# Kernel optimization log

Measured on AMD Instinct MI355X. Metric: run time of the kernel, lower is better.

## Reference

```python
import jax, jax.numpy as jnp
import numpy as np

B, S, DIM = 4, 2048, 1024
H, HD = 16, 64
MB = 16
NMB = S // MB
DEG, CP = 3, 8
NB = CP + DEG  # 11 basis functions
NKNOTS = CP + 1 + 2 * DEG  # 15
EPS = 1e-6
BASE_LR = 1.0


def bspline(x, knots, degree=DEG):
    # Cox-de Boor recursion; x: (...,), knots: (G,) uniform -> (..., G-1-degree)
    xk = x[..., None]
    G = knots.shape[0]
    b = ((xk >= knots[:-1]) & (xk < knots[1:])).astype(x.dtype)
    for k in range(1, degree + 1):
        left = (xk - knots[: G - 1 - k]) / (knots[k: G - 1] - knots[: G - 1 - k])
        right = (knots[k + 1: G] - xk) / (knots[k + 1: G] - knots[1: G - k])
        b = left * b[..., :-1] + right * b[..., 1:]
    return b


def ln_fwd(x, gamma, beta, eps=EPS):
    mu = x.mean(-1, keepdims=True)
    var = ((x - mu) ** 2).mean(-1, keepdims=True)
    x_hat = (x - mu) / jnp.sqrt(var + eps)
    return gamma * x_hat + beta


def ln_fused_l2_bwd(x, l2_target, gamma, beta, eps=EPS):
    mu = x.mean(-1, keepdims=True)
    var = ((x - mu) ** 2).mean(-1, keepdims=True)
    std = jnp.sqrt(var + eps)
    x_hat = (x - mu) / std
    grad_x_hat = (gamma * x_hat + beta - l2_target) * gamma
    z = (grad_x_hat - grad_x_hat.mean(-1, keepdims=True)
         - x_hat * (grad_x_hat * x_hat).mean(-1, keepdims=True)) / std
    return z


def apply_rope(t, ang):
    # t: (B,H,S,hd), ang: (S, hd//2) rotation angles
    cos, sin = jnp.cos(ang), jnp.sin(ang)
    t1, t2 = t[..., 0::2], t[..., 1::2]
    r1 = t1 * cos - t2 * sin
    r2 = t1 * sin + t2 * cos
    return jnp.stack([r1, r2], axis=-1).reshape(t.shape)


def setup_inputs() -> dict:
    key = jax.random.key(0)
    ks = jax.random.split(key, 8)
    s = 0.02
    x = jax.random.normal(ks[0], (B, S, DIM), dtype=jnp.float32)
    inv_freq = 1.0 / (10000.0 ** (jnp.arange(0, HD, 2, dtype=jnp.float32) / HD))
    pos_frequencies = jnp.arange(S, dtype=jnp.float32)[:, None] * inv_freq[None, :]
    Wq = jax.random.normal(ks[1], (DIM, DIM), dtype=jnp.float32) * s
    Wk = jax.random.normal(ks[2], (DIM, DIM), dtype=jnp.float32) * s
    Wv = jax.random.normal(ks[3], (DIM, DIM), dtype=jnp.float32) * s
    Wo = jax.random.normal(ks[4], (DIM, DIM), dtype=jnp.float32) * s
    lr_W = jax.random.normal(ks[5], (H, 1, DIM), dtype=jnp.float32) * s
    lr_b = jnp.zeros((H, 1), dtype=jnp.float32)
    g_scale = jnp.zeros((MB,), dtype=jnp.float32)
    ttt_gamma = jnp.ones((H, HD), dtype=jnp.float32)
    ttt_beta = jnp.zeros((H, HD), dtype=jnp.float32)
    post_w = jnp.ones((DIM,), dtype=jnp.float32)
    post_b = jnp.zeros((DIM,), dtype=jnp.float32)
    knots = jnp.linspace(-1.0, 1.0, NKNOTS, dtype=jnp.float32)
    coefficients = jax.random.normal(ks[6], (H, NB, HD), dtype=jnp.float32) * s
    return dict(x=x, pos_frequencies=pos_frequencies, Wq=Wq, Wk=Wk, Wv=Wv, Wo=Wo,
                lr_W=lr_W, lr_b=lr_b, g_scale=g_scale, ttt_gamma=ttt_gamma,
                ttt_beta=ttt_beta, post_w=post_w, post_b=post_b,
                coefficients=coefficients, knots=knots)


def reference(x, pos_frequencies, Wq, Wk, Wv, Wo, lr_W, lr_b, g_scale,
              ttt_gamma, ttt_beta, post_w, post_b, coefficients, knots):
    Bx, Sx = x.shape[:2]
    proj = lambda W: (x @ W.T).reshape(Bx, Sx, H, HD).transpose(0, 2, 1, 3)
    Q = apply_rope(proj(Wq), pos_frequencies)
    K = apply_rope(proj(Wk), pos_frequencies)
    V = apply_rope(proj(Wv), pos_frequencies)

    to_mb = lambda t: t.reshape(Bx, H, NMB, MB, HD).transpose(2, 0, 1, 3, 4)
    Qm, Km, Vm = to_mb(Q), to_mb(K), to_mb(V)  # (n,B,H,m,hd)

    # inner-loop learning rates (get_learning_rate)
    x4 = x.reshape(Bx, NMB, MB, DIM)
    lr = BASE_LR * jax.nn.sigmoid(
        jnp.einsum('bnkd,hd->bhnk', x4, lr_W[:, 0, :]) + lr_b.reshape(1, H, 1, 1)) / HD
    gs = jnp.clip(1.0 / jnp.arange(1, MB + 1, dtype=x.dtype) + g_scale, 0.0, None)
    eta = (lr * gs).transpose(2, 0, 1, 3)  # (n,B,H,m)

    gamma = ttt_gamma[None, :, None, :]
    beta = ttt_beta[None, :, None, :]
    W0 = jnp.broadcast_to(coefficients, (Bx, H, NB, HD))

    def step(W, inp):
        Qi, Ki, Vi, ei = inp  # (B,H,m,hd), eta (B,H,m)
        basK = bspline(Ki, knots)                      # (B,H,m,hd,nb)
        Zk = jax.nn.silu(Ki) + jnp.einsum('bhmdn,bhnd->bhmd', basK, W)
        gz = ln_fused_l2_bwd(Zk, Vi - Ki, gamma, beta)  # (B,H,m,hd)
        tok = jnp.einsum('bhm,bhmd,bhmdn->bhmnd', ei, gz, basK)
        cum = jnp.cumsum(tok, axis=2)                  # causal coeff-grad (B,H,m,nb,hd)
        basQ = bspline(Qi, knots)
        Zq = (jax.nn.silu(Qi)
              + jnp.einsum('bhmdn,bhnd->bhmd', basQ, W)
              - jnp.einsum('bhmdn,bhmnd->bhmd', basQ, cum))
        y = Qi + ln_fwd(Zq, gamma, beta)
        return W - cum[:, :, -1], y

    _, ys = jax.lax.scan(step, W0, (Qm, Km, Vm, eta))  # ys: (n,B,H,m,hd)
    out = ys.transpose(1, 0, 3, 2, 4).reshape(Bx, Sx, DIM)

    mu = out.mean(-1, keepdims=True)
    var = ((out - mu) ** 2).mean(-1, keepdims=True)
    out = (out - mu) / jnp.sqrt(var + EPS) * post_w + post_b
    return out @ Wo.T
```

## Files before the change

### kernel.cpp

```cpp
#include <hip/hip_runtime.h>
#include <stdint.h>


typedef unsigned short ushort_t;
typedef _Float16 f16x8 __attribute__((ext_vector_type(8)));
typedef float f32x4 __attribute__((ext_vector_type(4)));

__device__ __forceinline__ float bf2f(ushort_t u) {
    union { uint32_t i; float f; } v; v.i = ((uint32_t)u) << 16; return v.f;
}

__device__ __forceinline__ float fast_silu(float x) {
    const float e = __builtin_amdgcn_exp2f(-1.4426950408889634f * x);
    return x * __builtin_amdgcn_rcpf(1.0f + e);
}
__device__ __forceinline__ float fast_rsq(float x) {
    return __builtin_amdgcn_rsqf(x);
}

__device__ __forceinline__ void gl16(const ushort_t* g, ushort_t* l) {
    __builtin_amdgcn_global_load_lds(
        (const __attribute__((address_space(1))) void*)g,
        (__attribute__((address_space(3))) void*)l, 16, 0, 0);
}

template <int CTRL>
__device__ __forceinline__ float dpp_add(float v) {
    int p = __builtin_amdgcn_update_dpp(0, __float_as_int(v), CTRL, 0xF, 0xF, false);
    return v + __int_as_float(p);
}
__device__ __forceinline__ float wave_sum(float v) {
    v = dpp_add<0xB1>(v);
    v = dpp_add<0x4E>(v);
    v = dpp_add<0x141>(v);
    v = dpp_add<0x140>(v);
    v = dpp_add<0x142>(v);
    v = dpp_add<0x143>(v);
    return __int_as_float(__builtin_amdgcn_readlane(__float_as_int(v), 63));
}

__device__ __forceinline__ float rdl63(float v) {
    return __int_as_float(__builtin_amdgcn_readlane(__float_as_int(v), 63));
}

__device__ __forceinline__ void wave_sum6(float& s0, float& s1, float& s2,
                                          float& s3, float& s4, float& s5) {
    asm volatile(
        "s_nop 1\n\t"
        "v_add_f32_dpp %0, %0, %0 quad_perm:[1,0,3,2] row_mask:0xf bank_mask:0xf\n\t"
        "v_add_f32_dpp %1, %1, %1 quad_perm:[1,0,3,2] row_mask:0xf bank_mask:0xf\n\t"
        "v_add_f32_dpp %2, %2, %2 quad_perm:[1,0,3,2] row_mask:0xf bank_mask:0xf\n\t"
        "v_add_f32_dpp %3, %3, %3 quad_perm:[1,0,3,2] row_mask:0xf bank_mask:0xf\n\t"
        "v_add_f32_dpp %4, %4, %4 quad_perm:[1,0,3,2] row_mask:0xf bank_mask:0xf\n\t"
        "v_add_f32_dpp %5, %5, %5 quad_perm:[1,0,3,2] row_mask:0xf bank_mask:0xf\n\t"
        "v_add_f32_dpp %0, %0, %0 quad_perm:[2,3,0,1] row_mask:0xf bank_mask:0xf\n\t"
        "v_add_f32_dpp %1, %1, %1 quad_perm:[2,3,0,1] row_mask:0xf bank_mask:0xf\n\t"
        "v_add_f32_dpp %2, %2, %2 quad_perm:[2,3,0,1] row_mask:0xf bank_mask:0xf\n\t"
        "v_add_f32_dpp %3, %3, %3 quad_perm:[2,3,0,1] row_mask:0xf bank_mask:0xf\n\t"
        "v_add_f32_dpp %4, %4, %4 quad_perm:[2,3,0,1] row_mask:0xf bank_mask:0xf\n\t"
        "v_add_f32_dpp %5, %5, %5 quad_perm:[2,3,0,1] row_mask:0xf bank_mask:0xf\n\t"
        "v_add_f32_dpp %0, %0, %0 row_half_mirror row_mask:0xf bank_mask:0xf\n\t"
        "v_add_f32_dpp %1, %1, %1 row_half_mirror row_mask:0xf bank_mask:0xf\n\t"
        "v_add_f32_dpp %2, %2, %2 row_half_mirror row_mask:0xf bank_mask:0xf\n\t"
        "v_add_f32_dpp %3, %3, %3 row_half_mirror row_mask:0xf bank_mask:0xf\n\t"
        "v_add_f32_dpp %4, %4, %4 row_half_mirror row_mask:0xf bank_mask:0xf\n\t"
        "v_add_f32_dpp %5, %5, %5 row_half_mirror row_mask:0xf bank_mask:0xf\n\t"
        "v_add_f32_dpp %0, %0, %0 row_mirror row_mask:0xf bank_mask:0xf\n\t"
        "v_add_f32_dpp %1, %1, %1 row_mirror row_mask:0xf bank_mask:0xf\n\t"
        "v_add_f32_dpp %2, %2, %2 row_mirror row_mask:0xf bank_mask:0xf\n\t"
        "v_add_f32_dpp %3, %3, %3 row_mirror row_mask:0xf bank_mask:0xf\n\t"
        "v_add_f32_dpp %4, %4, %4 row_mirror row_mask:0xf bank_mask:0xf\n\t"
        "v_add_f32_dpp %5, %5, %5 row_mirror row_mask:0xf bank_mask:0xf\n\t"
        "v_add_f32_dpp %0, %0, %0 row_bcast:15 row_mask:0xf bank_mask:0xf bound_ctrl:0\n\t"
        "v_add_f32_dpp %1, %1, %1 row_bcast:15 row_mask:0xf bank_mask:0xf bound_ctrl:0\n\t"
        "v_add_f32_dpp %2, %2, %2 row_bcast:15 row_mask:0xf bank_mask:0xf bound_ctrl:0\n\t"
        "v_add_f32_dpp %3, %3, %3 row_bcast:15 row_mask:0xf bank_mask:0xf bound_ctrl:0\n\t"
        "v_add_f32_dpp %4, %4, %4 row_bcast:15 row_mask:0xf bank_mask:0xf bound_ctrl:0\n\t"
        "v_add_f32_dpp %5, %5, %5 row_bcast:15 row_mask:0xf bank_mask:0xf bound_ctrl:0\n\t"
        "v_add_f32_dpp %0, %0, %0 row_bcast:31 row_mask:0xf bank_mask:0xf bound_ctrl:0\n\t"
        "v_add_f32_dpp %1, %1, %1 row_bcast:31 row_mask:0xf bank_mask:0xf bound_ctrl:0\n\t"
        "v_add_f32_dpp %2, %2, %2 row_bcast:31 row_mask:0xf bank_mask:0xf bound_ctrl:0\n\t"
        "v_add_f32_dpp %3, %3, %3 row_bcast:31 row_mask:0xf bank_mask:0xf bound_ctrl:0\n\t"
        "v_add_f32_dpp %4, %4, %4 row_bcast:31 row_mask:0xf bank_mask:0xf bound_ctrl:0\n\t"
        "v_add_f32_dpp %5, %5, %5 row_bcast:31 row_mask:0xf bank_mask:0xf bound_ctrl:0"
        : "+v"(s0), "+v"(s1), "+v"(s2), "+v"(s3), "+v"(s4), "+v"(s5));
}

__device__ __forceinline__ void wave_sum2(float& s0, float& s1) {
    asm volatile(
        "s_nop 1\n\t"
        "v_add_f32_dpp %0, %0, %0 quad_perm:[1,0,3,2] row_mask:0xf bank_mask:0xf\n\t"
        "v_add_f32_dpp %1, %1, %1 quad_perm:[1,0,3,2] row_mask:0xf bank_mask:0xf\n\t"
        "s_nop 0\n\t"
        "v_add_f32_dpp %0, %0, %0 quad_perm:[2,3,0,1] row_mask:0xf bank_mask:0xf\n\t"
        "v_add_f32_dpp %1, %1, %1 quad_perm:[2,3,0,1] row_mask:0xf bank_mask:0xf\n\t"
        "s_nop 0\n\t"
        "v_add_f32_dpp %0, %0, %0 row_half_mirror row_mask:0xf bank_mask:0xf\n\t"
        "v_add_f32_dpp %1, %1, %1 row_half_mirror row_mask:0xf bank_mask:0xf\n\t"
        "s_nop 0\n\t"
        "v_add_f32_dpp %0, %0, %0 row_mirror row_mask:0xf bank_mask:0xf\n\t"
        "v_add_f32_dpp %1, %1, %1 row_mirror row_mask:0xf bank_mask:0xf\n\t"
        "s_nop 0\n\t"
        "v_add_f32_dpp %0, %0, %0 row_bcast:15 row_mask:0xf bank_mask:0xf bound_ctrl:0\n\t"
        "v_add_f32_dpp %1, %1, %1 row_bcast:15 row_mask:0xf bank_mask:0xf bound_ctrl:0\n\t"
        "s_nop 0\n\t"
        "v_add_f32_dpp %0, %0, %0 row_bcast:31 row_mask:0xf bank_mask:0xf bound_ctrl:0\n\t"
        "v_add_f32_dpp %1, %1, %1 row_bcast:31 row_mask:0xf bank_mask:0xf bound_ctrl:0"
        : "+v"(s0), "+v"(s1));
}

struct Bas4 { float n[4]; int row; };
__device__ __forceinline__ Bas4 bspline4(float x) {
    const float xp1 = x + 1.0f;
    const float s7 = xp1 * 7.0f;
    const float fi = floorf(s7);
    const bool valid = (fi >= 0.0f) && (fi <= 13.0f);
    const float fic = valid ? fi : 0.0f;
    const float t = s7 - fic;
    const float u = 1.0f - t;
    const float t2 = t * t;
    const float t3 = t2 * t;
    const float u3 = u * u * u;
    const float N0 = u3 * 0.16666666666666666f;
    const float N3 = t3 * 0.16666666666666666f;
    const float N1 = fmaf(0.5f, t3, 0.66666666666666666f - t2);
    const float N2 = 1.0f - N0 - N1 - N3;

    Bas4 r;
    const int i = (int)fic;
    const float nv[4] = {N0, N1, N2, N3};
#pragma unroll
    for (int tt = 0; tt < 4; ++tt) {
        const int j = i + tt - 3;
        const bool ok = valid && ((unsigned)j <= 10u);
        r.n[tt] = ok ? nv[tt] : 0.0f;
    }
    r.row = i;
    return r;
}

__device__ __forceinline__ void split16_body(
    const float* __restrict__ in, ushort_t* __restrict__ hi,
    ushort_t* __restrict__ lo, int i)
{
    const float4 f = reinterpret_cast<const float4*>(in)[i];
    union { _Float16 h[4]; ushort4 u; } hv, lv;
    hv.h[0] = (_Float16)f.x; hv.h[1] = (_Float16)f.y;
    hv.h[2] = (_Float16)f.z; hv.h[3] = (_Float16)f.w;
    lv.h[0] = (_Float16)(f.x - (float)hv.h[0]);
    lv.h[1] = (_Float16)(f.y - (float)hv.h[1]);
    lv.h[2] = (_Float16)(f.z - (float)hv.h[2]);
    lv.h[3] = (_Float16)(f.w - (float)hv.h[3]);
    reinterpret_cast<ushort4*>(hi)[i] = hv.u;
    reinterpret_cast<ushort4*>(lo)[i] = lv.u;
}

__device__ __forceinline__ void cast16_body(
    const float* __restrict__ in, ushort_t* __restrict__ out, int i)
{
    const float4 f = reinterpret_cast<const float4*>(in)[i];
    union { _Float16 h[4]; ushort4 u; } cv;
    cv.h[0] = (_Float16)f.x; cv.h[1] = (_Float16)f.y;
    cv.h[2] = (_Float16)f.z; cv.h[3] = (_Float16)f.w;
    reinterpret_cast<ushort4*>(out)[i] = cv.u;
}

__global__ __launch_bounds__(256) void prep_kernel(
    const float* __restrict__ x,
    const float* __restrict__ Wq, const float* __restrict__ Wk,
    const float* __restrict__ Wv,
    const float* __restrict__ lrW, const float* __restrict__ lrb,
    const float* __restrict__ gsc, const float* __restrict__ posf,
    ushort_t* __restrict__ xh, ushort_t* __restrict__ xl,
    ushort_t* __restrict__ Wq16, ushort_t* __restrict__ Wk16,
    ushort_t* __restrict__ Wv16,
    float* __restrict__ eta, float2* __restrict__ rtab)
{
    const int bid = blockIdx.x;
    const int tid = threadIdx.x;
    if (bid < 8192) {
        split16_body(x, xh, xl, bid * 256 + tid);
    } else if (bid < 9216) {
        cast16_body(Wq, Wq16, (bid - 8192) * 256 + tid);
    } else if (bid < 10240) {
        cast16_body(Wk, Wk16, (bid - 9216) * 256 + tid);
    } else if (bid < 11264) {
        cast16_body(Wv, Wv16, (bid - 10240) * 256 + tid);
    } else if (bid < 13312) {
        const int row = (bid - 11264) * 4 + (tid >> 6);
        const int lane = tid & 63;
        float xv[16];
#pragma unroll
        for (int i = 0; i < 16; ++i) xv[i] = x[(size_t)row * 1024 + lane + i * 64];
        const int b = row >> 11, s = row & 2047, n = s >> 4, m = s & 15;
        const float gs = fmaxf(1.0f / (float)(m + 1) + gsc[m], 0.0f);
        for (int h = 0; h < 16; ++h) {
            float acc = 0.0f;
#pragma unroll
            for (int i = 0; i < 16; ++i) acc += xv[i] * lrW[h * 1024 + lane + i * 64];
            acc = wave_sum(acc);
            if (lane == 0) {
                float sig = 1.0f / (1.0f + expf(-(acc + lrb[h])));
                eta[(((size_t)(b * 16 + h)) * 128 + n) * 16 + m] = (sig / 64.0f) * gs;
            }
        }
    } else {
        const int i = (bid - 13312) * 256 + tid;
        const float ang = posf[i];
        rtab[i] = make_float2(cosf(ang), sinf(ang));
    }
}

__global__ __launch_bounds__(256) void cast16_kernel(
    const float* __restrict__ in, ushort_t* __restrict__ out, int n4)
{
    const int i = blockIdx.x * 256 + threadIdx.x;
    if (i >= n4) return;
    cast16_body(in, out, i);
}

#define RAW_BAR()                                                              \
    __builtin_amdgcn_s_barrier();                                              \
    asm volatile("" ::: "memory");

__global__ __launch_bounds__(512) void qkv_rope_kernel(
    const ushort_t* __restrict__ xh, const ushort_t* __restrict__ xl,
    const ushort_t* __restrict__ Wq16, const ushort_t* __restrict__ Wk16,
    const ushort_t* __restrict__ Wv16,
    const float2* __restrict__ tab,
    float* __restrict__ Qb, float* __restrict__ Kb, float* __restrict__ Vb)
{
    const int cid = blockIdx.y * 64 + blockIdx.x;
    const int swz = (cid & 7) * 192 + (cid >> 3);
    const int rowbase = (swz & 63) * 128;
    const int colbase = (swz >> 6) * 128;
    const int sel = colbase >> 10;
    const ushort_t* WB = (sel == 0) ? Wq16 : (sel == 1) ? Wk16 : Wv16;
    float* dst = (sel == 0) ? Qb : (sel == 1) ? Kb : Vb;
    const int colm = colbase & 1023;

    __shared__ __align__(16) ushort_t Ash[2][4096];
    __shared__ __align__(16) ushort_t Asl[2][4096];
    __shared__ __align__(16) ushort_t Bsh[2][4096];
    const int tid = threadIdx.x;
    const int wv = tid >> 6, ln = tid & 63;
    const int l15 = ln & 15, lq = ln >> 4;
    const int lsw = lq ^ ((l15 >> 1) & 3);
    const int wm = wv >> 2, wn = wv & 3;
    const int srow = tid >> 2;
    const int skseg = (((tid & 3) ^ ((srow >> 1) & 3)) * 8);
    const ushort_t* gA_h = xh + (size_t)(rowbase + srow) * 1024 + skseg;
    const ushort_t* gA_l = xl + (size_t)(rowbase + srow) * 1024 + skseg;
    const ushort_t* gB   = WB + (size_t)(colm + srow) * 1024 + skseg;
    const int wlds = wv * 512;
    f32x4 acc[4][2] = {};

#define QK_STAGE(B, KO)                                                        \
    gl16(gA_h + (KO), &Ash[B][wlds]);                                          \
    gl16(gA_l + (KO), &Asl[B][wlds]);                                          \
    gl16(gB + (KO), &Bsh[B][wlds]);

#define QK_COMPUTE(B)                                                          \
    {                                                                          \
        f16x8 bh[2];                                                           \
        _Pragma("unroll")                                                      \
        for (int u = 0; u < 2; ++u) {                                          \
            const int br = (wn * 32 + u * 16 + l15) * 32 + lsw * 8;            \
            bh[u] = *reinterpret_cast<const f16x8*>(&Bsh[B][br]);              \
        }                                                                      \
        _Pragma("unroll")                                                      \
        for (int t = 0; t < 4; ++t) {                                          \
            const int ar = (wm * 64 + t * 16 + l15) * 32 + lsw * 8;            \
            const f16x8 ah = *reinterpret_cast<const f16x8*>(&Ash[B][ar]);     \
            const f16x8 al = *reinterpret_cast<const f16x8*>(&Asl[B][ar]);     \
            _Pragma("unroll")                                                  \
            for (int u = 0; u < 2; ++u) {                                      \
                acc[t][u] = __builtin_amdgcn_mfma_f32_16x16x32_f16(ah, bh[u], acc[t][u], 0, 0, 0); \
                acc[t][u] = __builtin_amdgcn_mfma_f32_16x16x32_f16(al, bh[u], acc[t][u], 0, 0, 0); \
            }                                                                  \
        }                                                                      \
    }

    QK_STAGE(0, 0)
    for (int k0 = 0; k0 < 1024; k0 += 64) {
        QK_STAGE(1, k0 + 32)
        asm volatile("s_waitcnt vmcnt(3)" ::: "memory");
        RAW_BAR()
        QK_COMPUTE(0)
        RAW_BAR()
        if (k0 + 64 < 1024) {
            QK_STAGE(0, k0 + 64)
            asm volatile("s_waitcnt vmcnt(3)" ::: "memory");
        } else {
            asm volatile("s_waitcnt vmcnt(0)" ::: "memory");
        }
        RAW_BAR()
        QK_COMPUTE(1)
        RAW_BAR()
    }
#undef QK_STAGE
#undef QK_COMPUTE

#pragma unroll
    for (int t = 0; t < 4; ++t)
#pragma unroll
        for (int u = 0; u < 2; ++u) {
            const int col = colm + wn * 32 + u * 16 + l15;
            const int d = col & 63, h = col >> 6;
            const int angidx = d >> 1;
            const int odd = d & 1;
#pragma unroll
            for (int r = 0; r < 4; ++r) {
                const int row = rowbase + wm * 64 + t * 16 + lq * 4 + r;
                const int b = row >> 11, s = row & 2047;
                const float2 cs = tab[s * 32 + angidx];
                const float own = acc[t][u][r];
                const float partner = __shfl_xor(own, 1, 64);
                const float res = odd ? (partner * cs.y + own * cs.x)
                                      : (own * cs.x - partner * cs.y);
                const int n = s >> 4, m = s & 15;
                dst[(((size_t)(b * 16 + h)) * 128 + n) * 1024 + m * 64 + d] = res;
            }
        }
}

__global__ __launch_bounds__(1024) void scan_kernel(
    const float* __restrict__ Qb, const float* __restrict__ Kb,
    const float* __restrict__ Vb, const float* __restrict__ eta,
    const float* __restrict__ tg, const float* __restrict__ tb,
    const float* __restrict__ coeff, float* __restrict__ out_pre)
{
    __shared__ __align__(16) float Wl[17 * 64];
    __shared__ __align__(16) float cum[16 * 17 * 64];
    __shared__ __align__(16) float Ucum[16 * 17 * 64];

    const int tid = threadIdx.x;
    const int m = tid >> 6, d = tid & 63;
    const int b = blockIdx.x >> 4, h = blockIdx.x & 15;

    const float gam = tg[h * 64 + d];
    const float bet = tb[h * 64 + d];
    const float gam2 = gam * gam;
    const float G = wave_sum(gam2);

    for (int i = tid; i < 1088; i += 1024)
        Wl[i] = (i >= 192 && i < 896) ? coeff[h * 704 + (i - 192)] : 0.0f;
    {
        const float4 z = {0.0f, 0.0f, 0.0f, 0.0f};
        float4* c4 = (float4*)cum;
        float4* u4 = (float4*)Ucum;
        for (int i = tid; i < 4352; i += 1024) { c4[i] = z; u4[i] = z; }
    }
    __syncthreads();

    const size_t base = ((size_t)(b * 16 + h)) * 131072;
    const float* Qp = Qb + base;
    const float* Kp = Kb + base;
    const float* Vp = Vb + base;
    const float* ep = eta + ((size_t)(b * 16 + h)) * 2048;

    float kf = Kp[tid], vf = Vp[tid], qf = Qp[tid], ei = ep[m];
    int rprev = 0;
    const int cb = m * 1088 + d;

    Bas4 bk = bspline4(kf);
    float szk = fast_silu(kf);
    float E = gam * (bet - (vf - kf));

    for (int n = 0; n < 128; ++n) {
        const int n1 = (n < 127) ? n + 1 : n;
        const float kfN = Kp[n1 * 1024 + tid];
        const float vfN = Vp[n1 * 1024 + tid];
        const float qfN = Qp[n1 * 1024 + tid];
        const float eiN = ep[n1 * 16 + m];

        float zk = szk;
        {
            const float* w = &Wl[bk.row * 64 + d];
            zk = fmaf(bk.n[0], w[0],   zk);
            zk = fmaf(bk.n[1], w[64],  zk);
            zk = fmaf(bk.n[2], w[128], zk);
            zk = fmaf(bk.n[3], w[192], zk);
        }

        float s0 = zk, s1 = zk * zk, s2 = gam2 * zk,
              s3 = gam2 * (zk * zk), s4 = E, s5 = E * zk;
        wave_sum6(s0, s1, s2, s3, s4, s5);
        const float r0 = rdl63(s0);
        const float r1 = rdl63(s1);
        const float r2 = rdl63(s2);
        const float r3 = rdl63(s3);
        const float r4 = rdl63(s4);
        const float r5 = rdl63(s5);

        const float mu = r0 * (1.0f / 64.0f);
        const float var = r1 * (1.0f / 64.0f) - mu * mu;
        const float rstd = fast_rsq(var + 1e-6f);
        const float xhat = (zk - mu) * rstd;
        const float gxh = gam2 * xhat + E;
        const float t1 = rstd * (r2 - mu * G) + r4;
        const float t2 = rstd * rstd * (r3 - 2.0f * mu * r2 + mu * mu * G)
                       + rstd * (r5 - mu * r4);
        const float gz = (gxh - t1 * (1.0f / 64.0f) - xhat * (t2 * (1.0f / 64.0f))) * rstd;

        const float tokf = ei * gz;
        {
            float* cz = &cum[cb + rprev * 64];
            cz[0] = 0.0f; cz[64] = 0.0f; cz[128] = 0.0f; cz[192] = 0.0f;
            float* cw = &cum[cb + bk.row * 64];
            cw[0]   = tokf * bk.n[0];
            cw[64]  = tokf * bk.n[1];
            cw[128] = tokf * bk.n[2];
            cw[192] = tokf * bk.n[3];
            rprev = bk.row;
        }
        __syncthreads();

        if (tid < 176) {
            float4* c4 = (float4*)cum;
            float4* u4 = (float4*)Ucum;
            float4* w4 = (float4*)Wl;
            float4 v[16];
#pragma unroll
            for (int mm = 0; mm < 16; ++mm) v[mm] = c4[mm * 272 + 48 + tid];
            float4 a = w4[48 + tid];
#pragma unroll
            for (int mm = 0; mm < 16; ++mm) {
                a.x -= v[mm].x; a.y -= v[mm].y; a.z -= v[mm].z; a.w -= v[mm].w;
                u4[mm * 272 + 48 + tid] = a;
            }
            w4[48 + tid] = a;
        }
        const Bas4 bq = bspline4(qf);
        float zq = fast_silu(qf);
        const Bas4 bkN = bspline4(kfN);
        const float szkN = fast_silu(kfN);
        const float EN = gam * (bet - (vfN - kfN));
        __syncthreads();

        {
            const float* u = &Ucum[cb + bq.row * 64];
            zq = fmaf(bq.n[0], u[0],   zq);
            zq = fmaf(bq.n[1], u[64],  zq);
            zq = fmaf(bq.n[2], u[128], zq);
            zq = fmaf(bq.n[3], u[192], zq);
        }

        float q0 = zq, q1 = zq * zq;
        wave_sum2(q0, q1);
        const float u1 = rdl63(q0);
        const float u2 = rdl63(q1);
        const float mu2 = u1 * (1.0f / 64.0f);
        const float var2 = u2 * (1.0f / 64.0f) - mu2 * mu2;
        const float rstd2 = fast_rsq(var2 + 1e-6f);
        const float y = qf + gam * (zq - mu2) * rstd2 + bet;
        out_pre[((size_t)b * 2048 + n * 16 + m) * 1024 + h * 64 + d] = y;

        kf = kfN; vf = vfN; qf = qfN; ei = eiN;
        bk = bkN; szk = szkN; E = EN;
    }
}

__global__ __launch_bounds__(256) void ln_kernel(
    const float* __restrict__ in, const float* __restrict__ pw,
    const float* __restrict__ pb, ushort_t* __restrict__ o16)
{
    const int row = blockIdx.x * 4 + (threadIdx.x >> 6);
    const int lane = threadIdx.x & 63;
    const float* r = in + (size_t)row * 1024;
    float v[16];
    float s1 = 0.0f, s2 = 0.0f;
#pragma unroll
    for (int i = 0; i < 16; ++i) {
        v[i] = r[lane + i * 64];
        s1 += v[i];
        s2 += v[i] * v[i];
    }
    s1 = wave_sum(s1);
    s2 = wave_sum(s2);
    const float mu = s1 * (1.0f / 1024.0f);
    const float var = s2 * (1.0f / 1024.0f) - mu * mu;
    const float rstd = rsqrtf(var + 1e-6f);
#pragma unroll
    for (int i = 0; i < 16; ++i) {
        const int c = lane + i * 64;
        const float o = (v[i] - mu) * rstd * pw[c] + pb[c];
        union { _Float16 h; ushort_t u; } cv;
        cv.h = (_Float16)o;
        o16[(size_t)row * 1024 + c] = cv.u;
    }
}

__global__ __launch_bounds__(512) void out_gemm_kernel(
    const ushort_t* __restrict__ Ag, const ushort_t* __restrict__ Bg,
    float* __restrict__ out)
{
    const int cid = blockIdx.y * 64 + blockIdx.x;
    const int swz = (cid & 7) * 64 + (cid >> 3);
    const int rowbase = (swz & 63) * 128;
    const int colbase = (swz >> 6) * 128;

    __shared__ __align__(16) ushort_t Ash[2][4096];
    __shared__ __align__(16) ushort_t Bsh[2][4096];
    const int tid = threadIdx.x;
    const int wv = tid >> 6, ln = tid & 63;
    const int l15 = ln & 15, lq = ln >> 4;
    const int lsw = lq ^ ((l15 >> 1) & 3);
    const int wm = wv >> 2, wn = wv & 3;
    const int srow = tid >> 2;
    const int skseg = (((tid & 3) ^ ((srow >> 1) & 3)) * 8);
    const ushort_t* gA = Ag + (size_t)(rowbase + srow) * 1024 + skseg;
    const ushort_t* gB = Bg + (size_t)(colbase + srow) * 1024 + skseg;
    const int wlds = wv * 512;
    f32x4 acc[4][2] = {};

#define OG_STAGE(B, KO)                                                        \
    gl16(gA + (KO), &Ash[B][wlds]);                                            \
    gl16(gB + (KO), &Bsh[B][wlds]);

#define OG_COMPUTE(B)                                                          \
    {                                                                          \
        f16x8 bh[2];                                                           \
        _Pragma("unroll")                                                      \
        for (int u = 0; u < 2; ++u) {                                          \
            const int br = (wn * 32 + u * 16 + l15) * 32 + lsw * 8;            \
            bh[u] = *reinterpret_cast<const f16x8*>(&Bsh[B][br]);              \
        }                                                                      \
        _Pragma("unroll")                                                      \
        for (int t = 0; t < 4; ++t) {                                          \
            const int ar = (wm * 64 + t * 16 + l15) * 32 + lsw * 8;            \
            const f16x8 ah = *reinterpret_cast<const f16x8*>(&Ash[B][ar]);     \
            _Pragma("unroll")                                                  \
            for (int u = 0; u < 2; ++u)                                        \
                acc[t][u] = __builtin_amdgcn_mfma_f32_16x16x32_f16(ah, bh[u], acc[t][u], 0, 0, 0); \
        }                                                                      \
    }

    OG_STAGE(0, 0)
    for (int k0 = 0; k0 < 1024; k0 += 64) {
        OG_STAGE(1, k0 + 32)
        asm volatile("s_waitcnt vmcnt(2)" ::: "memory");
        RAW_BAR()
        OG_COMPUTE(0)
        RAW_BAR()
        if (k0 + 64 < 1024) {
            OG_STAGE(0, k0 + 64)
            asm volatile("s_waitcnt vmcnt(2)" ::: "memory");
        } else {
            asm volatile("s_waitcnt vmcnt(0)" ::: "memory");
        }
        RAW_BAR()
        OG_COMPUTE(1)
        RAW_BAR()
    }
#undef OG_STAGE
#undef OG_COMPUTE

#pragma unroll
    for (int t = 0; t < 4; ++t)
#pragma unroll
        for (int u = 0; u < 2; ++u) {
            const int col = colbase + wn * 32 + u * 16 + l15;
#pragma unroll
            for (int r = 0; r < 4; ++r) {
                const int row = rowbase + wm * 64 + t * 16 + lq * 4 + r;
                out[(size_t)row * 1024 + col] = acc[t][u][r];
            }
        }
}

extern "C" void kernel_launch(void* const* d_in, const int* in_sizes, int n_in,
                              void* d_out, int out_size, void* d_ws, size_t ws_size,
                              hipStream_t stream) {
    const float* x    = (const float*)d_in[0];
    const float* posf = (const float*)d_in[1];
    const float* Wq   = (const float*)d_in[2];
    const float* Wk   = (const float*)d_in[3];
    const float* Wv   = (const float*)d_in[4];
    const float* Wo   = (const float*)d_in[5];
    const float* lrW  = (const float*)d_in[6];
    const float* lrb  = (const float*)d_in[7];
    const float* gsc  = (const float*)d_in[8];
    const float* tg   = (const float*)d_in[9];
    const float* tb   = (const float*)d_in[10];
    const float* pw   = (const float*)d_in[11];
    const float* pb   = (const float*)d_in[12];
    const float* coeff= (const float*)d_in[13];

    char* ws = (char*)d_ws;
    float*    Qb   = (float*)(ws);
    float*    Kb   = (float*)(ws + 33554432);
    float*    Vb   = (float*)(ws + 67108864);
    ushort_t* xh   = (ushort_t*)(ws + 100663296);
    ushort_t* xl   = (ushort_t*)(ws + 117440512);
    float*    outp = (float*)(ws + 100663296);
    float*    eta  = (float*)(ws + 134217728);
    ushort_t* Wq16 = (ushort_t*)(ws + 134742016);
    ushort_t* Wk16 = (ushort_t*)(ws + 136839168);
    ushort_t* Wv16 = (ushort_t*)(ws + 138936320);
    ushort_t* Wo16 = (ushort_t*)(ws + 147324928);
    ushort_t* ln16 = (ushort_t*)(ws);
    float2*   rtab = (float2*)(ws + 147324928);

    prep_kernel<<<13568, 256, 0, stream>>>(x, Wq, Wk, Wv, lrW, lrb, gsc, posf,
                                           xh, xl, Wq16, Wk16, Wv16, eta, rtab);
    qkv_rope_kernel<<<dim3(64, 24), 512, 0, stream>>>(xh, xl, Wq16, Wk16, Wv16,
                                                      rtab, Qb, Kb, Vb);
    cast16_kernel<<<1024, 256, 0, stream>>>(Wo, Wo16, 262144);
    scan_kernel<<<64, 1024, 0, stream>>>(Qb, Kb, Vb, eta, tg, tb, coeff, outp);
    ln_kernel<<<2048, 256, 0, stream>>>(outp, pw, pb, ln16);
    out_gemm_kernel<<<dim3(64, 8), 512, 0, stream>>>(ln16, Wo16, (float*)d_out);
}
```

Measured before the change: 543.6 us.

## Triple-buffer the QKV GEMM LDS pipeline with rotating stage pointers

The QKV+RoPE projection kernel goes from a two-stage to a three-stage shared-memory pipeline, so two K-slices of global-to-LDS loads are in flight while the current slice is computed. Buffers are rotated through pointers, and the vmcnt waits are adjusted to allow six outstanding loads. The aim is to hide more global load latency. The cost is 50% more LDS per block (about 72KB), which may reduce how many blocks fit on a CU, and the pointer-based addressing may add some index arithmetic.

```diff
diff --git a/kernel.cpp b/kernel.cpp
--- a/kernel.cpp
+++ b/kernel.cpp
@@ -5,10 +5,6 @@
 typedef unsigned short ushort_t;
 typedef _Float16 f16x8 __attribute__((ext_vector_type(8)));
 typedef float f32x4 __attribute__((ext_vector_type(4)));
-
-__device__ __forceinline__ float bf2f(ushort_t u) {
-    union { uint32_t i; float f; } v; v.i = ((uint32_t)u) << 16; return v.f;
-}
 
 __device__ __forceinline__ float fast_silu(float x) {
     const float e = __builtin_amdgcn_exp2f(-1.4426950408889634f * x);
@@ -239,9 +235,9 @@
     float* dst = (sel == 0) ? Qb : (sel == 1) ? Kb : Vb;
     const int colm = colbase & 1023;
 
-    __shared__ __align__(16) ushort_t Ash[2][4096];
-    __shared__ __align__(16) ushort_t Asl[2][4096];
-    __shared__ __align__(16) ushort_t Bsh[2][4096];
+    __shared__ __align__(16) ushort_t Ash[3][4096];
+    __shared__ __align__(16) ushort_t Asl[3][4096];
+    __shared__ __align__(16) ushort_t Bsh[3][4096];
     const int tid = threadIdx.x;
     const int wv = tid >> 6, ln = tid & 63;
     const int l15 = ln & 15, lq = ln >> 4;
@@ -255,51 +251,51 @@
     const int wlds = wv * 512;
     f32x4 acc[4][2] = {};
 
-#define QK_STAGE(B, KO)                                                        \
-    gl16(gA_h + (KO), &Ash[B][wlds]);                                          \
-    gl16(gA_l + (KO), &Asl[B][wlds]);                                          \
-    gl16(gB + (KO), &Bsh[B][wlds]);
-
-#define QK_COMPUTE(B)                                                          \
-    {                                                                          \
-        f16x8 bh[2];                                                           \
-        _Pragma("unroll")                                                      \
-        for (int u = 0; u < 2; ++u) {                                          \
-            const int br = (wn * 32 + u * 16 + l15) * 32 + lsw * 8;            \
-            bh[u] = *reinterpret_cast<const f16x8*>(&Bsh[B][br]);              \
-        }                                                                      \
-        _Pragma("unroll")                                                      \
-        for (int t = 0; t < 4; ++t) {                                          \
-            const int ar = (wm * 64 + t * 16 + l15) * 32 + lsw * 8;            \
-            const f16x8 ah = *reinterpret_cast<const f16x8*>(&Ash[B][ar]);     \
-            const f16x8 al = *reinterpret_cast<const f16x8*>(&Asl[B][ar]);     \
-            _Pragma("unroll")                                                  \
-            for (int u = 0; u < 2; ++u) {                                      \
-                acc[t][u] = __builtin_amdgcn_mfma_f32_16x16x32_f16(ah, bh[u], acc[t][u], 0, 0, 0); \
-                acc[t][u] = __builtin_amdgcn_mfma_f32_16x16x32_f16(al, bh[u], acc[t][u], 0, 0, 0); \
-            }                                                                  \
-        }                                                                      \
-    }
-
-    QK_STAGE(0, 0)
-    for (int k0 = 0; k0 < 1024; k0 += 64) {
-        QK_STAGE(1, k0 + 32)
-        asm volatile("s_waitcnt vmcnt(3)" ::: "memory");
-        RAW_BAR()
-        QK_COMPUTE(0)
-        RAW_BAR()
-        if (k0 + 64 < 1024) {
-            QK_STAGE(0, k0 + 64)
+    ushort_t *cAh = &Ash[0][0], *cAl = &Asl[0][0], *cB = &Bsh[0][0];
+    ushort_t *nAh = &Ash[1][0], *nAl = &Asl[1][0], *nB = &Bsh[1][0];
+    ushort_t *pAh = &Ash[2][0], *pAl = &Asl[2][0], *pB = &Bsh[2][0];
+
+    gl16(gA_h + 0,  cAh + wlds); gl16(gA_l + 0,  cAl + wlds); gl16(gB + 0,  cB + wlds);
+    gl16(gA_h + 32, nAh + wlds); gl16(gA_l + 32, nAl + wlds); gl16(gB + 32, nB + wlds);
+
+    for (int p = 0; p < 32; ++p) {
+        const int kn = (p + 2) * 32;
+        if (kn < 1024) {
+            gl16(gA_h + kn, pAh + wlds);
+            gl16(gA_l + kn, pAl + wlds);
+            gl16(gB + kn,   pB + wlds);
+            asm volatile("s_waitcnt vmcnt(6)" ::: "memory");
+        } else if (p == 30) {
             asm volatile("s_waitcnt vmcnt(3)" ::: "memory");
         } else {
             asm volatile("s_waitcnt vmcnt(0)" ::: "memory");
         }
         RAW_BAR()
-        QK_COMPUTE(1)
+        {
+            f16x8 bh[2];
+#pragma unroll
+            for (int u = 0; u < 2; ++u) {
+                const int br = (wn * 32 + u * 16 + l15) * 32 + lsw * 8;
+                bh[u] = *reinterpret_cast<const f16x8*>(&cB[br]);
+            }
+#pragma unroll
+            for (int t = 0; t < 4; ++t) {
+                const int ar = (wm * 64 + t * 16 + l15) * 32 + lsw * 8;
+                const f16x8 ah = *reinterpret_cast<const f16x8*>(&cAh[ar]);
+                const f16x8 al = *reinterpret_cast<const f16x8*>(&cAl[ar]);
+#pragma unroll
+                for (int u = 0; u < 2; ++u) {
+                    acc[t][u] = __builtin_amdgcn_mfma_f32_16x16x32_f16(ah, bh[u], acc[t][u], 0, 0, 0);
+                    acc[t][u] = __builtin_amdgcn_mfma_f32_16x16x32_f16(al, bh[u], acc[t][u], 0, 0, 0);
+                }
+            }
+        }
         RAW_BAR()
-    }
-#undef QK_STAGE
-#undef QK_COMPUTE
+        ushort_t* t0;
+        t0 = cAh; cAh = nAh; nAh = pAh; pAh = t0;
+        t0 = cAl; cAl = nAl; nAl = pAl; pAl = t0;
+        t0 = cB;  cB  = nB;  nB  = pB;  pB  = t0;
+    }
 
 #pragma unroll
     for (int t = 0; t < 4; ++t)
```

After: 537.0 us. Within noise of the previous version (-1.2%).
